# Kernel optimization log

Measured on AMD Instinct MI355X. Metric: run time of the kernel, lower is better.

The kernel has to match this reference:

```python
import jax, jax.numpy as jnp
import numpy as np

IMG_H, IMG_W = 240, 320
NEAR, FAR = 0.1, 10.0
CHUNK = 64  # triangles rasterized per scan step
CAM_K = np.array([[286.2057, 0.0, 162.6306],
                  [0.0, 286.7852, 121.0245],
                  [0.0, 0.0, 1.0]], np.float32)


def build_projection(cam, w, h, x0=0, y0=0, nc=NEAR, fc=FAR):
    q = -(fc + nc) / float(fc - nc)
    qn = -2.0 * fc * nc / float(fc - nc)
    proj = np.array([
        [2 * cam[0, 0] / w, -2 * cam[0, 1] / w, (-2 * cam[0, 2] + w + 2 * x0) / w, 0],
        [0, -2 * cam[1, 1] / h, (-2 * cam[1, 2] + h + 2 * y0) / h, 0],
        [0, 0, q, qn],
        [0, 0, -1, 0]], dtype=np.float64)
    proj[1, :] *= -1.0
    return jnp.asarray(proj.T, jnp.float32)


def vertex_normals(verts, faces):
    # per-face normal scattered to its vertices then renormalized
    # (equals dirt lighting.vertex_normals_pre_split on split meshes)
    v0, v1, v2 = verts[faces[:, 0]], verts[faces[:, 1]], verts[faces[:, 2]]
    fn = jnp.cross(v1 - v0, v2 - v0)
    fn = fn / jnp.maximum(jnp.linalg.norm(fn, axis=1, keepdims=True), 1e-12)
    vn = (jnp.zeros_like(verts)
          .at[faces[:, 0]].add(fn)
          .at[faces[:, 1]].add(fn)
          .at[faces[:, 2]].add(fn))
    return vn / jnp.maximum(jnp.linalg.norm(vn, axis=1, keepdims=True), 1e-12)


def transform_vertices(vertices, pose, faces, proj):
    vert_obj = jnp.concatenate([vertices, jnp.ones_like(vertices[:, -1:])], axis=1)  # [V,4]
    normals = vertex_normals(vert_obj[:, :3], faces)
    gl = jnp.array([[1., 0., 0.], [0., -1., 0.], [0., 0., -1.]], jnp.float32)
    rot = gl @ pose[:3, :3]
    # replicate the flat-list surgery: cam_pose[:3,:3]=gl@R, negate t_y, t_z
    cam_pose = pose.at[:3, :3].set(rot).at[1, 3].multiply(-1.0).at[2, 3].multiply(-1.0)
    view = cam_pose.T
    vert_cam = vert_obj @ view                                   # [V,4]
    vert_3d = vert_obj[:, :3] @ pose[:3, :3].T + pose[:3, 3]     # [V,3]
    vert_clip = vert_cam @ proj                                  # [V,4]
    return vert_obj, vert_3d, vert_clip, normals


def rasterise(vert_clip, colors, faces, H, W):
    # z-buffered triangle rasterization with perspective-correct barycentric
    # interpolation, processed in chunks of CHUNK triangles via lax.scan.
    eps = 1e-9
    wc = vert_clip[:, 3]
    inv_w = 1.0 / jnp.where(jnp.abs(wc) > eps, wc, eps)
    ndc = vert_clip[:, :3] * inv_w[:, None]
    px = (ndc[:, 0] + 1.0) * 0.5 * W   # screen x
    py = (1.0 - ndc[:, 1]) * 0.5 * H   # screen y (row 0 at top)
    pz = ndc[:, 2]

    tpx, tpy, tpz = px[faces], py[faces], pz[faces]   # [F,3]
    tiw = inv_w[faces]                                # [F,3]
    tcol = colors[faces]                              # [F,3,C]
    tval = jnp.all(wc[faces] > 1e-6, axis=1)          # all verts in front

    F = faces.shape[0]
    pad = (-F) % CHUNK
    def padf(a):
        if pad == 0:
            return a
        return jnp.concatenate([a, jnp.zeros((pad,) + a.shape[1:], a.dtype)], 0)
    tpx, tpy, tpz, tiw, tcol = padf(tpx), padf(tpy), padf(tpz), padf(tiw), padf(tcol)
    tval = padf(tval)
    n_steps = (F + pad) // CHUNK
    resh = lambda a: a.reshape((n_steps, CHUNK) + a.shape[1:])
    xs = tuple(map(resh, (tpx, tpy, tpz, tiw, tcol, tval)))

    Xg = (jnp.arange(W, dtype=jnp.float32) + 0.5)[None, :, None]  # pixel centers
    Yg = (jnp.arange(H, dtype=jnp.float32) + 0.5)[:, None, None]
    BIG = jnp.float32(1e9)

    def step(carry, chunk):
        zbuf, cbuf = carry
        cpx, cpy, cpz, ciw, ccol, cval = chunk
        ax, ay = cpx[:, 0], cpy[:, 0]
        bx, by = cpx[:, 1], cpy[:, 1]
        cx, cy = cpx[:, 2], cpy[:, 2]
        area = (bx - ax) * (cy - ay) - (by - ay) * (cx - ax)            # [Fc]
        inv_area = 1.0 / jnp.where(jnp.abs(area) > 1e-12, area, 1e-12)
        # normalized edge functions (barycentrics), [H,W,Fc]
        e0 = ((Xg - bx) * (cy - by) - (Yg - by) * (cx - bx)) * inv_area
        e1 = ((Xg - cx) * (ay - cy) - (Yg - cy) * (ax - cx)) * inv_area
        e2 = 1.0 - e0 - e1
        depth = e0 * cpz[:, 0] + e1 * cpz[:, 1] + e2 * cpz[:, 2]        # screen-linear z
        inside = ((e0 >= 0) & (e1 >= 0) & (e2 >= 0) & cval
                  & (jnp.abs(area) > 1e-12) & (depth >= -1.0) & (depth <= 1.0))
        dmask = jnp.where(inside, depth, BIG)
        best = jnp.argmin(dmask, axis=2)                                # [H,W]
        bidx = best[..., None]
        bdepth = jnp.take_along_axis(dmask, bidx, 2)[..., 0]
        take = bdepth < zbuf
        b0 = jnp.take_along_axis(e0, bidx, 2)[..., 0]
        b1 = jnp.take_along_axis(e1, bidx, 2)[..., 0]
        b2 = 1.0 - b0 - b1
        piw = jnp.stack([b0, b1, b2], -1) * ciw[best]                   # [H,W,3]
        den = jnp.sum(piw, -1, keepdims=True)
        den = jnp.where(jnp.abs(den) > 1e-12, den, 1e-12)
        col = jnp.einsum('hwk,hwkc->hwc', piw / den, ccol[best])        # persp-correct
        zbuf = jnp.where(take, bdepth, zbuf)
        cbuf = jnp.where(take[..., None], col, cbuf)
        return (zbuf, cbuf), None

    zbuf0 = jnp.full((H, W), BIG, jnp.float32)
    cbuf0 = jnp.zeros((H, W, colors.shape[1]), jnp.float32)
    (_, cbuf), _ = jax.lax.scan(jax.checkpoint(step), (zbuf0, cbuf0), xs)
    return cbuf


def setup_inputs() -> dict:
    key = jax.random.key(0)
    k1, k2 = jax.random.split(key)
    V, F = 12288, 4096
    vertices = 0.15 * jax.random.normal(k1, (1, V, 3), jnp.float32)
    faces = jax.random.randint(k2, (1, F, 3), 0, V, jnp.int32)
    pose = jnp.eye(4, dtype=jnp.float32).at[2, 3].set(0.6)  # object 0.6m in front
    return {"vertices": vertices, "faces": faces, "poses": pose[None]}


def reference(vertices, faces, poses):
    proj = build_projection(CAM_K, IMG_W, IMG_H)
    faces0 = jnp.asarray(faces[0], jnp.int32)
    vert_obj, vert_3d, vert_clip, normals = transform_vertices(vertices[0], poses[0], faces0, proj)
    colors = jnp.concatenate(
        [jnp.ones_like(vert_obj[:, :1]), vert_3d, normals, vert_obj], axis=1)  # [V,11]
    g = rasterise(vert_clip, colors, faces0, IMG_H, IMG_W)  # [H,W,11]
    return g[None]
```

## Files before the change

### kernel.cpp

```cpp
#include <hip/hip_runtime.h>
#include <math.h>

#pragma clang fp contract(off)

#define IMG_H 240
#define IMG_W 320
#define NPX   (IMG_H * IMG_W)
#define NCH   11
#define NCHP  12
#define NSLICE 8
#define CULL_M 1e-3f
#define EZ_M   1e-5f
#define NBIN   256

struct ProjM { float m[16]; };

__device__ __forceinline__ int zbin(float zm) {
  float t = fminf(fmaxf((zm + 1.0f) * 128.0f, 0.0f), 255.0f);
  int b = (int)t;
  if ((float)b * 0.0078125f - 1.0f > zm) b = (b > 0) ? b - 1 : 0;
  return b;
}

extern "C" __global__ void k_init(float* __restrict__ vnacc, int n3v,
                                  unsigned long long* __restrict__ zkey,
                                  int* __restrict__ hist) {
  int i = blockIdx.x * 256 + threadIdx.x;
  if (i < n3v) vnacc[i] = 0.0f;
  if (i < NPX) zkey[i] = ~0ull;
  if (i < NBIN) hist[i] = 0;
}

__device__ __forceinline__ void xform(float x, float y, float z,
                                      const float* __restrict__ pose,
                                      const ProjM& P,
                                      float& px, float& py, float& pz,
                                      float& iw, float& wc) {
  float c0 = ((x*pose[0]     + y*pose[1])     + z*pose[2])     + pose[3];
  float c1 = ((x*(-pose[4])  + y*(-pose[5]))  + z*(-pose[6]))  + (-pose[7]);
  float c2 = ((x*(-pose[8])  + y*(-pose[9]))  + z*(-pose[10])) + (-pose[11]);
  float c3 = ((x*pose[12]    + y*pose[13])    + z*pose[14])    + pose[15];
  float q0 = ((c0*P.m[0]  + c1*P.m[1])  + c2*P.m[2])  + c3*P.m[3];
  float q1 = ((c0*P.m[4]  + c1*P.m[5])  + c2*P.m[6])  + c3*P.m[7];
  float q2 = ((c0*P.m[8]  + c1*P.m[9])  + c2*P.m[10]) + c3*P.m[11];
  float q3 = ((c0*P.m[12] + c1*P.m[13]) + c2*P.m[14]) + c3*P.m[15];
  wc = q3;
  float denw = (fabsf(wc) > 1e-9f) ? wc : 1e-9f;
  iw = 1.0f / denw;
  float ndx = q0 * iw, ndy = q1 * iw;
  pz = q2 * iw;
  px = ((ndx + 1.0f) * 0.5f) * (float)IMG_W;
  py = ((1.0f - ndy) * 0.5f) * (float)IMG_H;
}

extern "C" __global__ void k_face(const float* __restrict__ verts,
                                  const int* __restrict__ faces,
                                  const float* __restrict__ pose,
                                  ProjM P,
                                  float* __restrict__ vnacc,
                                  float4* __restrict__ frec,
                                  float4* __restrict__ fbb,
                                  float4* __restrict__ fe,
                                  int4*  __restrict__ fidx,
                                  float* __restrict__ fzmin,
                                  int*   __restrict__ hist, int F) {
  int f = blockIdx.x * 64 + threadIdx.x;
  if (f >= F) return;
  int i0 = faces[3*f+0], i1 = faces[3*f+1], i2 = faces[3*f+2];
  float x0 = verts[3*i0+0], y0 = verts[3*i0+1], z0 = verts[3*i0+2];
  float x1 = verts[3*i1+0], y1 = verts[3*i1+1], z1 = verts[3*i1+2];
  float x2 = verts[3*i2+0], y2 = verts[3*i2+1], z2 = verts[3*i2+2];

  {
    float ux = x1 - x0, uy = y1 - y0, uz = z1 - z0;
    float vx = x2 - x0, vy = y2 - y0, vz = z2 - z0;
    float fx = uy*vz - uz*vy;
    float fy = uz*vx - ux*vz;
    float fz = ux*vy - uy*vx;
    float n = sqrtf((fx*fx + fy*fy) + fz*fz);
    float d = fmaxf(n, 1e-12f);
    fx = fx / d; fy = fy / d; fz = fz / d;
    atomicAdd(&vnacc[3*i0+0], fx); atomicAdd(&vnacc[3*i0+1], fy); atomicAdd(&vnacc[3*i0+2], fz);
    atomicAdd(&vnacc[3*i1+0], fx); atomicAdd(&vnacc[3*i1+1], fy); atomicAdd(&vnacc[3*i1+2], fz);
    atomicAdd(&vnacc[3*i2+0], fx); atomicAdd(&vnacc[3*i2+1], fy); atomicAdd(&vnacc[3*i2+2], fz);
  }

  float ax, ay, pz0, iw0, w0;  xform(x0, y0, z0, pose, P, ax, ay, pz0, iw0, w0);
  float bx, by, pz1, iw1, w1;  xform(x1, y1, z1, pose, P, bx, by, pz1, iw1, w1);
  float cx, cy, pz2, iw2, w2;  xform(x2, y2, z2, pose, P, cx, cy, pz2, iw2, w2);

  float area = (bx - ax) * (cy - ay) - (by - ay) * (cx - ax);
  float inva = 1.0f / ((fabsf(area) > 1e-12f) ? area : 1e-12f);
  bool valid = (w0 > 1e-6f) && (w1 > 1e-6f) && (w2 > 1e-6f) && (fabsf(area) > 1e-12f);
  float rax = 2.0f*cx - ax, ray = 2.0f*cy - ay;
  float rbx = 2.0f*cx - bx, rby = 2.0f*cy - by;
  float minx = fminf(cx, fminf(rax, rbx)), maxx = fmaxf(cx, fmaxf(rax, rbx));
  float miny = fminf(cy, fminf(ray, rby)), maxy = fmaxf(cy, fmaxf(ray, rby));
  frec[4*f+0] = make_float4(bx, by, cy - by, cx - bx);
  frec[4*f+1] = make_float4(cx, cy, ay - cy, ax - cx);
  frec[4*f+2] = make_float4(inva, pz0, pz1, pz2);
  frec[4*f+3] = make_float4(iw0, iw1, iw2, 0.0f);
  fbb[f] = valid ? make_float4(minx, maxx, miny, maxy)
                 : make_float4(1e30f, -1e30f, 1e30f, -1e30f);
  fidx[f] = make_int4(i0, i1, i2, 0);

  float zm = valid ? fminf(pz0, fminf(pz1, pz2)) : __builtin_huge_valf();
  fzmin[f] = zm;
  atomicAdd(&hist[zbin(zm)], 1);

  {
    double dbx = bx, dby = by, dcx = cx, dcy = cy, dax = ax, day = ay;
    double dinv = (double)inva;
    double d0 = dcy - dby, d1 = dcx - dbx;
    double d2 = day - dcy, d3 = dax - dcx;
    double a0 = d0 * dinv, b0 = -d1 * dinv, c0 = (dby * d1 - dbx * d0) * dinv;
    double a1 = d2 * dinv, b1 = -d3 * dinv, c1 = (dcy * d3 - dcx * d2) * dinv;
    fe[2*f+0] = make_float4((float)a0, (float)b0, (float)c0, 0.0f);
    fe[2*f+1] = make_float4((float)a1, (float)b1, (float)c1, 0.0f);
  }
}

extern "C" __global__ void k_scan(const int* __restrict__ hist,
                                  int* __restrict__ binoff) {
  __shared__ int s[NBIN];
  int t = threadIdx.x;
  int v = hist[t];
  s[t] = v;
  __syncthreads();
  for (int o = 1; o < NBIN; o <<= 1) {
    int x = (t >= o) ? s[t - o] : 0;
    __syncthreads();
    s[t] += x;
    __syncthreads();
  }
  binoff[t] = s[t] - v;
}

extern "C" __global__ void k_scatter(const float* __restrict__ fzmin,
                                     int* __restrict__ binoff,
                                     const float4* __restrict__ fbb,
                                     const float4* __restrict__ fe,
                                     const float4* __restrict__ frec,
                                     int*   __restrict__ forig,
                                     float* __restrict__ szmin,
                                     float* __restrict__ smon,
                                     float4* __restrict__ fbbs,
                                     float4* __restrict__ fes,
                                     float4* __restrict__ frecs, int F) {
  int f = blockIdx.x * 256 + threadIdx.x;
  if (f >= F) return;
  float zm = fzmin[f];
  int b = zbin(zm);
  int pos = atomicAdd(&binoff[b], 1);
  forig[pos] = f;
  szmin[pos] = zm;
  smon[pos]  = (float)b * 0.0078125f - 1.0f;
  fbbs[pos]  = fbb[f];
  fes[2*pos+0] = fe[2*f+0];
  fes[2*pos+1] = fe[2*f+1];
  frecs[4*pos+0] = frec[4*f+0];
  frecs[4*pos+1] = frec[4*f+1];
  frecs[4*pos+2] = frec[4*f+2];
  frecs[4*pos+3] = frec[4*f+3];
}

extern "C" __global__ void k_vertex(const float* __restrict__ verts,
                                    const float* __restrict__ vnacc,
                                    const float* __restrict__ pose,
                                    float4* __restrict__ colors, int V) {
  int i = blockIdx.x * 64 + threadIdx.x;
  if (i >= V) return;
  float x = verts[3*i+0], y = verts[3*i+1], z = verts[3*i+2];

  float nx = vnacc[3*i+0], ny = vnacc[3*i+1], nz = vnacc[3*i+2];
  float nn = sqrtf((nx*nx + ny*ny) + nz*nz);
  float nm = fmaxf(nn, 1e-12f);
  nx = nx / nm; ny = ny / nm; nz = nz / nm;

  float v3x = ((x*pose[0] + y*pose[1]) + z*pose[2])  + pose[3];
  float v3y = ((x*pose[4] + y*pose[5]) + z*pose[6])  + pose[7];
  float v3z = ((x*pose[8] + y*pose[9]) + z*pose[10]) + pose[11];

  colors[3*i+0] = make_float4(1.0f, v3x, v3y, v3z);
  colors[3*i+1] = make_float4(nx, ny, nz, x);
  colors[3*i+2] = make_float4(y, z, 1.0f, 0.0f);
}

extern "C" __global__ __launch_bounds__(256)
void k_rasterA(const float4* __restrict__ frecs,
               const float4* __restrict__ fbbs,
               const float4* __restrict__ fes,
               const int*    __restrict__ forig,
               const float*  __restrict__ szmin,
               const float*  __restrict__ smon,
               unsigned long long* __restrict__ zkey,
               int F) {
  int t = threadIdx.x;
  int wave = t >> 6;
  int lane = t & 63;
  int sx = (wave & 1) * 8, sy = (wave >> 1) * 8;
  int pxi = blockIdx.x * 16 + sx + (lane & 7);
  int pyi = blockIdx.y * 16 + sy + (lane >> 3);
  float X = (float)pxi + 0.5f;
  float Y = (float)pyi + 0.5f;
  float tXlo = (float)(blockIdx.x * 16 + sx) + 0.5f, tXhi = tXlo + 7.0f;
  float tYlo = (float)(blockIdx.y * 16 + sy) + 0.5f, tYhi = tYlo + 7.0f;
  size_t pix = (size_t)pyi * IMG_W + pxi;

  float bestd = 1.0f + 1.0e-3f;
  int   besti = -1;

  int nchunk = (F + 63) >> 6;
  for (int c = blockIdx.z; c < nchunk; c += NSLICE) {
    int base = c << 6;

    float pb = bestd;
    {
      unsigned long long k = __hip_atomic_load(&zkey[pix], __ATOMIC_RELAXED,
                                               __HIP_MEMORY_SCOPE_AGENT);
      if (k != ~0ull) {
        unsigned int ub = (unsigned int)(k >> 32);
        unsigned int fb = (ub & 0x80000000u) ? (ub & 0x7FFFFFFFu) : ~ub;
        pb = fminf(pb, __uint_as_float(fb));
      }
    }
    float pbm = pb;
    #pragma unroll
    for (int o = 32; o > 0; o >>= 1) pbm = fmaxf(pbm, __shfl_xor(pbm, o));

    if (pbm <= smon[base] - EZ_M) break;

    int i = base + lane;
    float szlane = __builtin_huge_valf();
    int   folane = 0;
    bool ov = false;
    if (i < F) {
      szlane = szmin[i];
      folane = forig[i];
      if (szlane < pbm + EZ_M) {
        float4 bb = fbbs[i];
        ov = (bb.x - 1.0f <= tXhi) && (bb.y + 1.0f >= tXlo) &&
             (bb.z - 1.0f <= tYhi) && (bb.w + 1.0f >= tYlo);
        if (ov) {
          float4 E0 = fes[2*i+0];
          float4 E1 = fes[2*i+1];
          float pa0 = E0.x * tXlo, pb0 = E0.x * tXhi;
          float qa0 = E0.y * tYlo, qb0 = E0.y * tYhi;
          float e0mx = (fmaxf(pa0, pb0) + fmaxf(qa0, qb0)) + E0.z;
          float pa1 = E1.x * tXlo, pb1 = E1.x * tXhi;
          float qa1 = E1.y * tYlo, qb1 = E1.y * tYhi;
          float e1mx = (fmaxf(pa1, pb1) + fmaxf(qa1, qb1)) + E1.z;
          float e0mn = (fminf(pa0, pb0) + fminf(qa0, qb0)) + E0.z;
          float e1mn = (fminf(pa1, pb1) + fminf(qa1, qb1)) + E1.z;
          float e2mx = (1.0f - e0mn) - e1mn;
          ov = (e0mx >= -CULL_M) && (e1mx >= -CULL_M) && (e2mx >= -CULL_M);
        }
      }
    }
    unsigned long long mask = __ballot(ov);
    bool improved = false;

    while (mask) {
      int j = __builtin_ctzll(mask);
      mask &= mask - 1;
      float zminf = __shfl(szlane, j);
      if (__ballot(bestd > zminf - EZ_M) == 0ull) continue;
      int jj = __builtin_amdgcn_readfirstlane(base + j);
      int ju = __builtin_amdgcn_readfirstlane(__shfl(folane, j));
      const float4* fr = frecs + (size_t)jj * 4;
      float4 A = fr[0];
      float4 B = fr[1];
      float4 C = fr[2];
      float t0 = (X - A.x) * A.z;
      float t1 = (Y - A.y) * A.w;
      float e0 = (t0 - t1) * C.x;
      float t2 = (X - B.x) * B.z;
      float t3 = (Y - B.y) * B.w;
      float e1 = (t2 - t3) * C.x;
      float e2 = (1.0f - e0) - e1;
      float depth = ((e0 * C.y) + (e1 * C.z)) + (e2 * C.w);
      bool inside = (e0 >= 0.0f) && (e1 >= 0.0f) && (e2 >= 0.0f) &&
                    (depth >= -1.0f) && (depth <= 1.0f);
      if (inside && (depth < bestd || (depth == bestd && ju < besti))) {
        bestd = depth; besti = ju; improved = true;
      }
    }

    if (improved && bestd <= pb) {
      unsigned int ub = __float_as_uint(bestd);
      ub = (ub & 0x80000000u) ? ~ub : (ub | 0x80000000u);
      unsigned long long key = ((unsigned long long)ub << 32) | (unsigned int)besti;
      atomicMin(&zkey[pix], key);
    }
  }
}

extern "C" __global__ __launch_bounds__(256)
void k_resolve(const unsigned long long* __restrict__ zkey,
               const float4* __restrict__ frec,
               const float4* __restrict__ colors,
               const int4* __restrict__ fidx,
               float* __restrict__ out) {
  __shared__ float sOut[256 * NCH];
  int t = threadIdx.x;
  int p = blockIdx.x * 256 + t;
  int pyi = p / IMG_W, pxi = p - pyi * IMG_W;
  float X = (float)pxi + 0.5f;
  float Y = (float)pyi + 0.5f;
  unsigned long long key = zkey[p];

  float oc[NCH];
  if (key != ~0ull) {
    int besti = (int)(key & 0xFFFFFFFFu);
    const float4* fr = frec + (size_t)besti * 4;
    float4 A = fr[0], B = fr[1], C = fr[2], D = fr[3];
    float t0 = (X - A.x) * A.z;
    float t1 = (Y - A.y) * A.w;
    float e0 = (t0 - t1) * C.x;
    float t2 = (X - B.x) * B.z;
    float t3 = (Y - B.y) * B.w;
    float e1 = (t2 - t3) * C.x;
    float b2 = (1.0f - e0) - e1;
    float p0 = e0 * D.x, p1 = e1 * D.y, p2 = b2 * D.z;
    float den = (p0 + p1) + p2;
    if (!(fabsf(den) > 1e-12f)) den = 1e-12f;
    float u0 = p0 / den, u1 = p1 / den, u2 = p2 / den;
    int4 vi = fidx[besti];
    float c0v[NCHP], c1v[NCHP], c2v[NCHP];
    #pragma unroll
    for (int k = 0; k < 3; ++k) {
      *(float4*)(c0v + 4*k) = colors[3*vi.x + k];
      *(float4*)(c1v + 4*k) = colors[3*vi.y + k];
      *(float4*)(c2v + 4*k) = colors[3*vi.z + k];
    }
    #pragma unroll
    for (int ch = 0; ch < NCH; ++ch)
      oc[ch] = (u0 * c0v[ch] + u1 * c1v[ch]) + u2 * c2v[ch];
  } else {
    #pragma unroll
    for (int ch = 0; ch < NCH; ++ch) oc[ch] = 0.0f;
  }
  #pragma unroll
  for (int ch = 0; ch < NCH; ++ch) sOut[t * NCH + ch] = oc[ch];
  __syncthreads();
  float4* o4 = (float4*)(out + (size_t)blockIdx.x * 256 * NCH);
  const float4* s4 = (const float4*)sOut;
  #pragma unroll
  for (int k = 0; k < 3; ++k) {
    int idx = t + k * 256;
    if (idx < 704) o4[idx] = s4[idx];
  }
}

extern "C" void kernel_launch(void* const* d_in, const int* in_sizes, int n_in,
                              void* d_out, int out_size, void* d_ws, size_t ws_size,
                              hipStream_t stream) {
  const float* verts = (const float*)d_in[0];
  const int*   faces = (const int*)d_in[1];
  const float* pose  = (const float*)d_in[2];
  float* out = (float*)d_out;
  int V = in_sizes[0] / 3;
  int F = in_sizes[1] / 3;

  float* ws = (float*)d_ws;
  size_t o = 0;
  auto alloc = [&](size_t n) { size_t r = o; o += (n + 3) & ~(size_t)3; return r; };
  size_t o_zk   = alloc((size_t)2 * NPX);
  size_t o_vn   = alloc((size_t)3 * V);
  size_t o_col  = alloc((size_t)NCHP * V);
  size_t o_fr   = alloc((size_t)16 * F);
  size_t o_bb   = alloc((size_t)4 * F);
  size_t o_fe   = alloc((size_t)8 * F);
  size_t o_fi   = alloc((size_t)4 * F);
  size_t o_fz   = alloc((size_t)F);
  size_t o_hist = alloc((size_t)NBIN);
  size_t o_boff = alloc((size_t)NBIN);
  size_t o_fo   = alloc((size_t)F);
  size_t o_sz   = alloc((size_t)F);
  size_t o_sm   = alloc((size_t)F);
  size_t o_bbs  = alloc((size_t)4 * F);
  size_t o_fes  = alloc((size_t)8 * F);
  size_t o_frs  = alloc((size_t)16 * F);
  unsigned long long* zkey = (unsigned long long*)(ws + o_zk);
  float*  vnacc = ws + o_vn;
  float4* col   = (float4*)(ws + o_col);
  float4* frec  = (float4*)(ws + o_fr);
  float4* fbb   = (float4*)(ws + o_bb);
  float4* fe    = (float4*)(ws + o_fe);
  int4*   fidx  = (int4*)(ws + o_fi);
  float*  fzmin = ws + o_fz;
  int*    hist  = (int*)(ws + o_hist);
  int*    boff  = (int*)(ws + o_boff);
  int*    forig = (int*)(ws + o_fo);
  float*  szmin = ws + o_sz;
  float*  smon  = ws + o_sm;
  float4* fbbs  = (float4*)(ws + o_bbs);
  float4* fes   = (float4*)(ws + o_fes);
  float4* frecs = (float4*)(ws + o_frs);

  double fxd = 286.2057, sd = 0.0, cxd = 162.6306;
  double fyd = 286.7852, cyd = 121.0245;
  double wd = IMG_W, hd = IMG_H, ncd = 0.1, fcd = 10.0;
  double q  = -(fcd + ncd) / (fcd - ncd);
  double qn = -2.0 * fcd * ncd / (fcd - ncd);
  double Pd[16] = {
    2.0*fxd/wd, -2.0*sd/wd, (-2.0*cxd + wd)/wd, 0.0,
    0.0,        2.0*fyd/hd, (2.0*cyd - hd)/hd, -0.0,
    0.0,        0.0,        q,                  qn,
    0.0,        0.0,       -1.0,                0.0 };
  ProjM P;
  for (int i = 0; i < 16; ++i) P.m[i] = (float)Pd[i];

  int n3v = 3 * V;
  int initN = (NPX > n3v) ? NPX : n3v;
  k_init<<<(initN + 255) / 256, 256, 0, stream>>>(vnacc, n3v, zkey, hist);
  k_face<<<(F + 63) / 64, 64, 0, stream>>>(verts, faces, pose, P, vnacc,
                                           frec, fbb, fe, fidx, fzmin, hist, F);
  k_scan<<<1, NBIN, 0, stream>>>(hist, boff);
  k_scatter<<<(F + 255) / 256, 256, 0, stream>>>(fzmin, boff, fbb, fe, frec,
                                                 forig, szmin, smon, fbbs, fes,
                                                 frecs, F);
  k_vertex<<<(V + 63) / 64, 64, 0, stream>>>(verts, vnacc, pose, col, V);
  dim3 g(IMG_W / 16, IMG_H / 16, NSLICE);
  k_rasterA<<<g, 256, 0, stream>>>(frecs, fbbs, fes, forig, szmin, smon, zkey, F);
  k_resolve<<<NPX / 256, 256, 0, stream>>>(zkey, frec, col, fidx, out);
}
```

Measured before the change: 103.7 us.

## Fuse scan into scatter, drop vertex kernel, and test two triangles per raster iteration

Several changes land together to cut kernel launches. The separate prefix-scan kernel is folded into the scatter kernel, where each block redundantly recomputes the 256-bin scan in shared memory and adds a per-bin atomic counter. The z-key buffer clear moves into the face kernel, which now launches 256-thread blocks over max(NPX, F). The per-vertex color kernel is removed, and the resolve kernel now computes normals and transformed positions on the fly from verts and vnacc. Separately, the raster inner loop handles two candidate triangles per iteration with a combined early-out ballot, which adds instruction-level parallelism but means a pair is culled only when both triangles can be skipped.

```diff
diff --git a/kernel.cpp b/kernel.cpp
--- a/kernel.cpp
+++ b/kernel.cpp
@@ -7,7 +7,6 @@
 #define IMG_W 320
 #define NPX   (IMG_H * IMG_W)
 #define NCH   11
-#define NCHP  12
 #define NSLICE 8
 #define CULL_M 1e-3f
 #define EZ_M   1e-5f
@@ -23,12 +22,11 @@
 }
 
 extern "C" __global__ void k_init(float* __restrict__ vnacc, int n3v,
-                                  unsigned long long* __restrict__ zkey,
-                                  int* __restrict__ hist) {
+                                  int* __restrict__ hist,
+                                  int* __restrict__ binctr) {
   int i = blockIdx.x * 256 + threadIdx.x;
   if (i < n3v) vnacc[i] = 0.0f;
-  if (i < NPX) zkey[i] = ~0ull;
-  if (i < NBIN) hist[i] = 0;
+  if (i < NBIN) { hist[i] = 0; binctr[i] = 0; }
 }
 
 __device__ __forceinline__ void xform(float x, float y, float z,
@@ -63,8 +61,11 @@
                                   float4* __restrict__ fe,
                                   int4*  __restrict__ fidx,
                                   float* __restrict__ fzmin,
-                                  int*   __restrict__ hist, int F) {
-  int f = blockIdx.x * 64 + threadIdx.x;
+                                  int*   __restrict__ hist,
+                                  unsigned long long* __restrict__ zkey,
+                                  int F) {
+  int f = blockIdx.x * 256 + threadIdx.x;
+  if (f < NPX) zkey[f] = ~0ull;
   if (f >= F) return;
   int i0 = faces[3*f+0], i1 = faces[3*f+1], i2 = faces[3*f+2];
   float x0 = verts[3*i0+0], y0 = verts[3*i0+1], z0 = verts[3*i0+2];
@@ -120,9 +121,20 @@
   }
 }
 
-extern "C" __global__ void k_scan(const int* __restrict__ hist,
-                                  int* __restrict__ binoff) {
+extern "C" __global__ void k_scatter(const float* __restrict__ fzmin,
+                                     const int* __restrict__ hist,
+                                     int* __restrict__ binctr,
+                                     const float4* __restrict__ fbb,
+                                     const float4* __restrict__ fe,
+                                     const float4* __restrict__ frec,
+                                     int*   __restrict__ forig,
+                                     float* __restrict__ szmin,
+                                     float* __restrict__ smon,
+                                     float4* __restrict__ fbbs,
+                                     float4* __restrict__ fes,
+                                     float4* __restrict__ frecs, int F) {
   __shared__ int s[NBIN];
+  __shared__ int ex[NBIN];
   int t = threadIdx.x;
   int v = hist[t];
   s[t] = v;
@@ -133,25 +145,14 @@
     s[t] += x;
     __syncthreads();
   }
-  binoff[t] = s[t] - v;
-}
-
-extern "C" __global__ void k_scatter(const float* __restrict__ fzmin,
-                                     int* __restrict__ binoff,
-                                     const float4* __restrict__ fbb,
-                                     const float4* __restrict__ fe,
-                                     const float4* __restrict__ frec,
-                                     int*   __restrict__ forig,
-                                     float* __restrict__ szmin,
-                                     float* __restrict__ smon,
-                                     float4* __restrict__ fbbs,
-                                     float4* __restrict__ fes,
-                                     float4* __restrict__ frecs, int F) {
-  int f = blockIdx.x * 256 + threadIdx.x;
+  ex[t] = s[t] - v;
+  __syncthreads();
+
+  int f = blockIdx.x * 256 + t;
   if (f >= F) return;
   float zm = fzmin[f];
   int b = zbin(zm);
-  int pos = atomicAdd(&binoff[b], 1);
+  int pos = ex[b] + atomicAdd(&binctr[b], 1);
   forig[pos] = f;
   szmin[pos] = zm;
   smon[pos]  = (float)b * 0.0078125f - 1.0f;
@@ -162,28 +163,6 @@
   frecs[4*pos+1] = frec[4*f+1];
   frecs[4*pos+2] = frec[4*f+2];
   frecs[4*pos+3] = frec[4*f+3];
-}
-
-extern "C" __global__ void k_vertex(const float* __restrict__ verts,
-                                    const float* __restrict__ vnacc,
-                                    const float* __restrict__ pose,
-                                    float4* __restrict__ colors, int V) {
-  int i = blockIdx.x * 64 + threadIdx.x;
-  if (i >= V) return;
-  float x = verts[3*i+0], y = verts[3*i+1], z = verts[3*i+2];
-
-  float nx = vnacc[3*i+0], ny = vnacc[3*i+1], nz = vnacc[3*i+2];
-  float nn = sqrtf((nx*nx + ny*ny) + nz*nz);
-  float nm = fmaxf(nn, 1e-12f);
-  nx = nx / nm; ny = ny / nm; nz = nz / nm;
-
-  float v3x = ((x*pose[0] + y*pose[1]) + z*pose[2])  + pose[3];
-  float v3y = ((x*pose[4] + y*pose[5]) + z*pose[6])  + pose[7];
-  float v3z = ((x*pose[8] + y*pose[9]) + z*pose[10]) + pose[11];
-
-  colors[3*i+0] = make_float4(1.0f, v3x, v3y, v3z);
-  colors[3*i+1] = make_float4(nx, ny, nz, x);
-  colors[3*i+2] = make_float4(y, z, 1.0f, 0.0f);
 }
 
 extern "C" __global__ __launch_bounds__(256)
@@ -261,28 +240,55 @@
     bool improved = false;
 
     while (mask) {
-      int j = __builtin_ctzll(mask);
+      int j0 = __builtin_ctzll(mask);
       mask &= mask - 1;
-      float zminf = __shfl(szlane, j);
-      if (__ballot(bestd > zminf - EZ_M) == 0ull) continue;
-      int jj = __builtin_amdgcn_readfirstlane(base + j);
-      int ju = __builtin_amdgcn_readfirstlane(__shfl(folane, j));
-      const float4* fr = frecs + (size_t)jj * 4;
-      float4 A = fr[0];
-      float4 B = fr[1];
-      float4 C = fr[2];
-      float t0 = (X - A.x) * A.z;
-      float t1 = (Y - A.y) * A.w;
-      float e0 = (t0 - t1) * C.x;
-      float t2 = (X - B.x) * B.z;
-      float t3 = (Y - B.y) * B.w;
-      float e1 = (t2 - t3) * C.x;
-      float e2 = (1.0f - e0) - e1;
-      float depth = ((e0 * C.y) + (e1 * C.z)) + (e2 * C.w);
-      bool inside = (e0 >= 0.0f) && (e1 >= 0.0f) && (e2 >= 0.0f) &&
-                    (depth >= -1.0f) && (depth <= 1.0f);
-      if (inside && (depth < bestd || (depth == bestd && ju < besti))) {
-        bestd = depth; besti = ju; improved = true;
+      bool two = (mask != 0ull);
+      int j1 = two ? __builtin_ctzll(mask) : j0;
+      if (two) mask &= mask - 1;
+
+      float zm0 = __shfl(szlane, j0);
+      float zm1 = __shfl(szlane, j1);
+      float zmg = fminf(zm0, zm1);
+      if (__ballot(bestd > zmg - EZ_M) == 0ull) continue;
+
+      int jj0 = __builtin_amdgcn_readfirstlane(base + j0);
+      int jj1 = __builtin_amdgcn_readfirstlane(base + j1);
+      int fo0 = __builtin_amdgcn_readfirstlane(__shfl(folane, j0));
+      int fo1 = __builtin_amdgcn_readfirstlane(__shfl(folane, j1));
+      const float4* fr0 = frecs + (size_t)jj0 * 4;
+      const float4* fr1 = frecs + (size_t)jj1 * 4;
+      float4 A0 = fr0[0], B0 = fr0[1], C0 = fr0[2];
+      float4 A1 = fr1[0], B1 = fr1[1], C1 = fr1[2];
+
+      {
+        float t0 = (X - A0.x) * A0.z;
+        float t1 = (Y - A0.y) * A0.w;
+        float e0 = (t0 - t1) * C0.x;
+        float t2 = (X - B0.x) * B0.z;
+        float t3 = (Y - B0.y) * B0.w;
+        float e1 = (t2 - t3) * C0.x;
+        float e2 = (1.0f - e0) - e1;
+        float depth = ((e0 * C0.y) + (e1 * C0.z)) + (e2 * C0.w);
+        bool inside = (e0 >= 0.0f) && (e1 >= 0.0f) && (e2 >= 0.0f) &&
+                      (depth >= -1.0f) && (depth <= 1.0f);
+        if (inside && (depth < bestd || (depth == bestd && fo0 < besti))) {
+          bestd = depth; besti = fo0; improved = true;
+        }
+      }
+      if (two) {
+        float t0 = (X - A1.x) * A1.z;
+        float t1 = (Y - A1.y) * A1.w;
+        float e0 = (t0 - t1) * C1.x;
+        float t2 = (X - B1.x) * B1.z;
+        float t3 = (Y - B1.y) * B1.w;
+        float e1 = (t2 - t3) * C1.x;
+        float e2 = (1.0f - e0) - e1;
+        float depth = ((e0 * C1.y) + (e1 * C1.z)) + (e2 * C1.w);
+        bool inside = (e0 >= 0.0f) && (e1 >= 0.0f) && (e2 >= 0.0f) &&
+                      (depth >= -1.0f) && (depth <= 1.0f);
+        if (inside && (depth < bestd || (depth == bestd && fo1 < besti))) {
+          bestd = depth; besti = fo1; improved = true;
+        }
       }
     }
 
@@ -298,8 +304,10 @@
 extern "C" __global__ __launch_bounds__(256)
 void k_resolve(const unsigned long long* __restrict__ zkey,
                const float4* __restrict__ frec,
-               const float4* __restrict__ colors,
                const int4* __restrict__ fidx,
+               const float* __restrict__ verts,
+               const float* __restrict__ vnacc,
+               const float* __restrict__ pose,
                float* __restrict__ out) {
   __shared__ float sOut[256 * NCH];
   int t = threadIdx.x;
@@ -326,16 +334,27 @@
     if (!(fabsf(den) > 1e-12f)) den = 1e-12f;
     float u0 = p0 / den, u1 = p1 / den, u2 = p2 / den;
     int4 vi = fidx[besti];
-    float c0v[NCHP], c1v[NCHP], c2v[NCHP];
+
+    float cv[3][NCH];
+    int vids[3] = { vi.x, vi.y, vi.z };
     #pragma unroll
     for (int k = 0; k < 3; ++k) {
-      *(float4*)(c0v + 4*k) = colors[3*vi.x + k];
-      *(float4*)(c1v + 4*k) = colors[3*vi.y + k];
-      *(float4*)(c2v + 4*k) = colors[3*vi.z + k];
+      int id = vids[k];
+      float x = verts[3*id+0], y = verts[3*id+1], z = verts[3*id+2];
+      float nx = vnacc[3*id+0], ny = vnacc[3*id+1], nz = vnacc[3*id+2];
+      float nn = sqrtf((nx*nx + ny*ny) + nz*nz);
+      float nm = fmaxf(nn, 1e-12f);
+      nx = nx / nm; ny = ny / nm; nz = nz / nm;
+      float v3x = ((x*pose[0] + y*pose[1]) + z*pose[2])  + pose[3];
+      float v3y = ((x*pose[4] + y*pose[5]) + z*pose[6])  + pose[7];
+      float v3z = ((x*pose[8] + y*pose[9]) + z*pose[10]) + pose[11];
+      cv[k][0] = 1.0f;  cv[k][1] = v3x; cv[k][2] = v3y; cv[k][3] = v3z;
+      cv[k][4] = nx;    cv[k][5] = ny;  cv[k][6] = nz;
+      cv[k][7] = x;     cv[k][8] = y;   cv[k][9] = z;   cv[k][10] = 1.0f;
     }
     #pragma unroll
     for (int ch = 0; ch < NCH; ++ch)
-      oc[ch] = (u0 * c0v[ch] + u1 * c1v[ch]) + u2 * c2v[ch];
+      oc[ch] = (u0 * cv[0][ch] + u1 * cv[1][ch]) + u2 * cv[2][ch];
   } else {
     #pragma unroll
     for (int ch = 0; ch < NCH; ++ch) oc[ch] = 0.0f;
@@ -367,14 +386,13 @@
   auto alloc = [&](size_t n) { size_t r = o; o += (n + 3) & ~(size_t)3; return r; };
   size_t o_zk   = alloc((size_t)2 * NPX);
   size_t o_vn   = alloc((size_t)3 * V);
-  size_t o_col  = alloc((size_t)NCHP * V);
   size_t o_fr   = alloc((size_t)16 * F);
   size_t o_bb   = alloc((size_t)4 * F);
   size_t o_fe   = alloc((size_t)8 * F);
   size_t o_fi   = alloc((size_t)4 * F);
   size_t o_fz   = alloc((size_t)F);
   size_t o_hist = alloc((size_t)NBIN);
-  size_t o_boff = alloc((size_t)NBIN);
+  size_t o_bc   = alloc((size_t)NBIN);
   size_t o_fo   = alloc((size_t)F);
   size_t o_sz   = alloc((size_t)F);
   size_t o_sm   = alloc((size_t)F);
@@ -383,14 +401,13 @@
   size_t o_frs  = alloc((size_t)16 * F);
   unsigned long long* zkey = (unsigned long long*)(ws + o_zk);
   float*  vnacc = ws + o_vn;
-  float4* col   = (float4*)(ws + o_col);
   float4* frec  = (float4*)(ws + o_fr);
   float4* fbb   = (float4*)(ws + o_bb);
   float4* fe    = (float4*)(ws + o_fe);
   int4*   fidx  = (int4*)(ws + o_fi);
   float*  fzmin = ws + o_fz;
   int*    hist  = (int*)(ws + o_hist);
-  int*    boff  = (int*)(ws + o_boff);
+  int*    binctr= (int*)(ws + o_bc);
   int*    forig = (int*)(ws + o_fo);
   float*  szmin = ws + o_sz;
   float*  smon  = ws + o_sm;
@@ -412,16 +429,15 @@
   for (int i = 0; i < 16; ++i) P.m[i] = (float)Pd[i];
 
   int n3v = 3 * V;
-  int initN = (NPX > n3v) ? NPX : n3v;
-  k_init<<<(initN + 255) / 256, 256, 0, stream>>>(vnacc, n3v, zkey, hist);
-  k_face<<<(F + 63) / 64, 64, 0, stream>>>(verts, faces, pose, P, vnacc,
-                                           frec, fbb, fe, fidx, fzmin, hist, F);
-  k_scan<<<1, NBIN, 0, stream>>>(hist, boff);
-  k_scatter<<<(F + 255) / 256, 256, 0, stream>>>(fzmin, boff, fbb, fe, frec,
-                                                 forig, szmin, smon, fbbs, fes,
-                                                 frecs, F);
-  k_vertex<<<(V + 63) / 64, 64, 0, stream>>>(verts, vnacc, pose, col, V);
+  k_init<<<(n3v + 255) / 256, 256, 0, stream>>>(vnacc, n3v, hist, binctr);
+  int gface = ((NPX > F ? NPX : F) + 255) / 256;
+  k_face<<<gface, 256, 0, stream>>>(verts, faces, pose, P, vnacc,
+                                    frec, fbb, fe, fidx, fzmin, hist, zkey, F);
+  k_scatter<<<(F + 255) / 256, 256, 0, stream>>>(fzmin, hist, binctr, fbb, fe,
+                                                 frec, forig, szmin, smon,
+                                                 fbbs, fes, frecs, F);
   dim3 g(IMG_W / 16, IMG_H / 16, NSLICE);
   k_rasterA<<<g, 256, 0, stream>>>(frecs, fbbs, fes, forig, szmin, smon, zkey, F);
-  k_resolve<<<NPX / 256, 256, 0, stream>>>(zkey, frec, col, fidx, out);
-}
+  k_resolve<<<NPX / 256, 256, 0, stream>>>(zkey, frec, fidx, verts, vnacc,
+                                           pose, out);
+}
```

Result: no change. 104.2 us (+0.4%).
